# Kernel tuning notes

Measured on AMD Instinct MI355X. Metric: run time of the kernel, lower is better.

The kernel has to match this reference:

```python
import jax, jax.numpy as jnp
import numpy as np

D_MODEL = 1024
N_HEADS = 16
FEAT_DIM = 16   # q/k head dim before feature-map expansion
V_DIM = 64      # v head dim = d_model / n_heads
EPS = 1e-12


def taylor_exp(x):
    """2nd-order Taylor approx feature map of exp(q^T k / sqrt(d)).
    x: (b, h, l, d) -> (b, h, l, 1 + d + d^2)
    f(x) = [1, x / d^{1/4}, vec(x x^T) / (sqrt(2) * sqrt(d))]
    """
    d = x.shape[-1]
    rd = jnp.sqrt(jnp.float32(d))          # sqrt(d)
    rrd = jnp.sqrt(rd)                     # d^{1/4}
    r2 = jnp.sqrt(jnp.float32(2.0))
    x2 = (x[..., :, None] * x[..., None, :]).reshape(*x.shape[:-1], d * d) / r2
    ones = jnp.ones(x.shape[:-1] + (1,), dtype=x.dtype)
    return jnp.concatenate([ones, x / rrd, x2 / rd], axis=-1)


def setup_inputs() -> dict:
    key = jax.random.key(0)
    k0, k1, k2, k3, k4 = jax.random.split(key, 5)
    b, l = 2, 2048
    scale = 1.0 / np.sqrt(D_MODEL)
    return {
        "hidden_states": jax.random.normal(k0, (b, l, D_MODEL), dtype=jnp.float32),
        "Wq": jax.random.normal(k1, (D_MODEL, N_HEADS * FEAT_DIM), dtype=jnp.float32) * scale,
        "Wk": jax.random.normal(k2, (D_MODEL, N_HEADS * FEAT_DIM), dtype=jnp.float32) * scale,
        "Wv": jax.random.normal(k3, (D_MODEL, N_HEADS * V_DIM), dtype=jnp.float32) * scale,
        "Wo": jax.random.normal(k4, (N_HEADS * V_DIM, D_MODEL), dtype=jnp.float32) * scale,
    }


def reference(hidden_states, Wq, Wk, Wv, Wo):
    b, l, _ = hidden_states.shape
    # projections -> (b, h, l, d)
    q = (hidden_states @ Wq).reshape(b, l, N_HEADS, FEAT_DIM).transpose(0, 2, 1, 3)
    k = (hidden_states @ Wk).reshape(b, l, N_HEADS, FEAT_DIM).transpose(0, 2, 1, 3)
    v = (hidden_states @ Wv).reshape(b, l, N_HEADS, V_DIM).transpose(0, 2, 1, 3)

    qf = taylor_exp(q)  # (b, h, l, 273)
    kf = taylor_exp(k)

    # causal linear attention (naive parallel form used by the torch module)
    A = jnp.einsum('bhnf,bhmf->bhnm', qf, kf)
    A = jnp.tril(A)
    y = jnp.einsum('bhnm,bhme->bhne', A, v)
    # denominator: q_f . cumsum(k_f)
    z = 1.0 / (jnp.einsum('bhlf,bhlf->bhl', qf, jnp.cumsum(kf, axis=2)) + EPS)
    y = y * z[..., None]

    out = y.transpose(0, 2, 1, 3).reshape(b, l, N_HEADS * V_DIM) @ Wo
    return out
```

## Files before the change

kernel.cpp:

```cpp
#include <hip/hip_runtime.h>
#include <hip/hip_bf16.h>

#define BATCH 2
#define LSEQ 2048
#define DMODEL 1024
#define NH 16
#define DQK 16
#define DV 64
#define FDIM 273
#define CHUNK 128
#define NCH (LSEQ / CHUNK)
#define ROWS (BATCH * LSEQ)
#define NBH (BATCH * NH)
#define NBC (NBH * NCH)
#define QKVW 1536
#define C2 0.17677669529663687f

typedef short bf16x8 __attribute__((ext_vector_type(8)));
typedef float f32x4 __attribute__((ext_vector_type(4)));

__device__ __forceinline__ unsigned short f2bf(float f) {
  __hip_bfloat16 h = __float2bfloat16(f);
  unsigned short u; __builtin_memcpy(&u, &h, 2); return u;
}
__device__ __forceinline__ float bf2f(unsigned short u) {
  unsigned int v = (unsigned int)u << 16; float f; __builtin_memcpy(&f, &v, 4); return f;
}

__device__ __forceinline__ void storeC(float* C, size_t off, float v) { C[off] = v; }
__device__ __forceinline__ void storeC(unsigned short* C, size_t off, float v) {
  C[off] = f2bf(v);
}

__global__ __launch_bounds__(256) void prep(
    const float* __restrict__ hs,
    const float* __restrict__ Wq, const float* __restrict__ Wk,
    const float* __restrict__ Wv, const float* __restrict__ Wo,
    unsigned short* __restrict__ hsb,
    unsigned short* __restrict__ wqt, unsigned short* __restrict__ wkt,
    unsigned short* __restrict__ wvt, unsigned short* __restrict__ wot) {
  __shared__ float t[32][33];
  if (blockIdx.z == 4) {
    int bid = blockIdx.y * 32 + blockIdx.x;
    const float4* in4 = (const float4*)hs;
#pragma unroll
    for (int k = 0; k < 4; k++) {
      int i = bid * 1024 + k * 256 + threadIdx.x;
      float4 v = in4[i];
      ushort4 o = {f2bf(v.x), f2bf(v.y), f2bf(v.z), f2bf(v.w)};
      ((ushort4*)hsb)[i] = o;
    }
    return;
  }
  const float* W; unsigned short* Wt; int N;
  switch (blockIdx.z) {
    case 0: W = Wq; Wt = wqt; N = 256; break;
    case 1: W = Wk; Wt = wkt; N = 256; break;
    case 2: W = Wv; Wt = wvt; N = 1024; break;
    default: W = Wo; Wt = wot; N = 1024; break;
  }
  const int nb = blockIdx.x * 32;
  if (nb >= N) return;
  const int kb = blockIdx.y * 32;
  const int tx = threadIdx.x & 31, ty4 = (threadIdx.x >> 5) * 4;
#pragma unroll
  for (int r = 0; r < 4; r++)
    t[ty4 + r][tx] = W[(size_t)(kb + ty4 + r) * N + nb + tx];
  __syncthreads();
#pragma unroll
  for (int r = 0; r < 4; r++)
    Wt[(size_t)(nb + ty4 + r) * DMODEL + kb + tx] = f2bf(t[tx][ty4 + r]);
}

template <typename CT>
__global__ __launch_bounds__(256) void gemm_mfma64(
    const unsigned short* __restrict__ A, const unsigned short* __restrict__ Bt,
    CT* __restrict__ C, int M, int N, int K) {
  __shared__ unsigned short As[256 * 8];
  __shared__ unsigned short Bs[512 * 8];
  const int tid = threadIdx.x;
  const int bm = blockIdx.y * 64, bn = blockIdx.x * 128;
  const int lane = tid & 63;
  const int w = tid >> 6;
  const int qr = (w >> 1) * 32, qc = (w & 1) * 64;
  f32x4 acc[2][4] = {};

  for (int k0 = 0; k0 < K; k0 += 32) {
#pragma unroll
    for (int j = 0; j < 3; ++j) {
      int c = j * 256 + tid;
      const unsigned short* gp;
      unsigned short* lp;
      if (c < 256) {
        int cc = c;
        int row = ((cc >> 6) << 4) + (cc & 15);
        int kh = (cc >> 4) & 3;
        gp = A + (size_t)(bm + row) * K + k0 + kh * 8; lp = As + cc * 8;
      } else {
        int cc = c - 256;
        int row = ((cc >> 6) << 4) + (cc & 15);
        int kh = (cc >> 4) & 3;
        gp = Bt + (size_t)(bn + row) * K + k0 + kh * 8; lp = Bs + cc * 8;
      }
      __builtin_amdgcn_global_load_lds(
          (const __attribute__((address_space(1))) unsigned int*)(const void*)gp,
          (__attribute__((address_space(3))) unsigned int*)lp, 16, 0, 0);
    }
    __syncthreads();
    bf16x8 a[2], b[4];
#pragma unroll
    for (int i = 0; i < 2; ++i)
      a[i] = *(const bf16x8*)(As + ((qr >> 4) + i) * 512 + lane * 8);
#pragma unroll
    for (int i = 0; i < 4; ++i)
      b[i] = *(const bf16x8*)(Bs + ((qc >> 4) + i) * 512 + lane * 8);
#pragma unroll
    for (int i = 0; i < 2; ++i)
#pragma unroll
      for (int jj = 0; jj < 4; ++jj)
        acc[i][jj] = __builtin_amdgcn_mfma_f32_16x16x32_bf16(a[i], b[jj], acc[i][jj], 0, 0, 0);
    __syncthreads();
  }
  const int cn = lane & 15, r0 = (lane >> 4) * 4;
#pragma unroll
  for (int i = 0; i < 2; ++i)
#pragma unroll
    for (int jj = 0; jj < 4; ++jj) {
      size_t base = (size_t)(bm + qr + i * 16 + r0) * N + bn + qc + jj * 16 + cn;
#pragma unroll
      for (int r = 0; r < 4; ++r) storeC(C, base + (size_t)r * N, acc[i][jj][r]);
    }
}

__device__ __forceinline__ void stage_Vp(const unsigned short* __restrict__ qkvb,
                                         int row0, int h, int tid, short* Vp) {
#pragma unroll
  for (int it = 0; it < 4; it++) {
    int t = it * 256 + tid;
    int j = t >> 3, e0 = (t & 7) * 8;
    bf16x8 v8 = *(const bf16x8*)(qkvb + (size_t)(row0 + j) * QKVW + 512 + h * 64 + e0);
    int jg = j >> 3, jj = j & 7;
#pragma unroll
    for (int u = 0; u < 8; u++) {
      int e = e0 + u;
      Vp[((e >> 4) * 4 + (jg >> 2)) * 512 + ((jg & 3) * 16 + (e & 15)) * 8 + jj] =
          v8[u];
    }
  }
  {
    int n = tid & 15, jgrp = tid >> 4;
    bf16x8 v8;
#pragma unroll
    for (int u = 0; u < 8; u++) v8[u] = (n == 0) ? (short)0x3F80 : (short)0;
    *(bf16x8*)(Vp + (16 + (jgrp >> 2)) * 512 + ((jgrp & 3) * 16 + n) * 8) = v8;
  }
}

__global__ __launch_bounds__(256) void chunk_sums_mfma(
    const unsigned short* __restrict__ qkvb, unsigned short* __restrict__ Sfrag) {
  const int c = blockIdx.x, bh = blockIdx.y;
  const int b = bh >> 4, h = bh & 15;
  const int tid = threadIdx.x;
  const int lane = tid & 63, w = tid >> 6;
  const int row0 = b * LSEQ + c * CHUNK;

  __shared__ float ksT[16 * 132];
  __shared__ short SH[56 * 512];
  short* Vp = SH;
  short* Kf0 = SH + 20 * 512;
  short* Kf1 = SH + 38 * 512;

  {
    int i = tid >> 1, d0 = (tid & 1) * 8;
    bf16x8 k8 = *(const bf16x8*)(qkvb + (size_t)(row0 + i) * QKVW + 256 + h * 16 + d0);
#pragma unroll
    for (int j = 0; j < 8; j++) ksT[(d0 + j) * 132 + i] = bf2f((unsigned short)k8[j]);
  }
  stage_Vp(qkvb, row0, h, tid, Vp);
  __syncthreads();

  auto gen = [&](int kt, short* dst) {
    for (int o = tid; o < 1152; o += 256) {
      int mt = o >> 6, w6 = o & 63;
      int kh = w6 >> 4, m = w6 & 15;
      int f = mt * 16 + m;
      int i0 = kt * 32 + kh * 8;
      bf16x8 v8;
      if (f == 0) {
#pragma unroll
        for (int j = 0; j < 8; j++) v8[j] = (short)0x3F80;
      } else if (f < 17) {
        const float* ka = &ksT[(f - 1) * 132 + i0];
        float4 a0 = *(const float4*)ka, a1 = *(const float4*)(ka + 4);
        v8[0] = (short)f2bf(0.5f * a0.x); v8[1] = (short)f2bf(0.5f * a0.y);
        v8[2] = (short)f2bf(0.5f * a0.z); v8[3] = (short)f2bf(0.5f * a0.w);
        v8[4] = (short)f2bf(0.5f * a1.x); v8[5] = (short)f2bf(0.5f * a1.y);
        v8[6] = (short)f2bf(0.5f * a1.z); v8[7] = (short)f2bf(0.5f * a1.w);
      } else if (f < FDIM) {
        int ix = f - 17;
        const float* ka = &ksT[(ix >> 4) * 132 + i0];
        const float* kb2 = &ksT[(ix & 15) * 132 + i0];
        float4 a0 = *(const float4*)ka, a1 = *(const float4*)(ka + 4);
        float4 b0 = *(const float4*)kb2, b1 = *(const float4*)(kb2 + 4);
        v8[0] = (short)f2bf(C2 * a0.x * b0.x); v8[1] = (short)f2bf(C2 * a0.y * b0.y);
        v8[2] = (short)f2bf(C2 * a0.z * b0.z); v8[3] = (short)f2bf(C2 * a0.w * b0.w);
        v8[4] = (short)f2bf(C2 * a1.x * b1.x); v8[5] = (short)f2bf(C2 * a1.y * b1.y);
        v8[6] = (short)f2bf(C2 * a1.z * b1.z); v8[7] = (short)f2bf(C2 * a1.w * b1.w);
      } else {
#pragma unroll
        for (int j = 0; j < 8; j++) v8[j] = 0;
      }
      *(bf16x8*)(dst + mt * 512 + (kh * 16 + m) * 8) = v8;
    }
  };

  gen(0, Kf0);
  __syncthreads();

  f32x4 acc[5][5] = {};
  const int nmt = (w < 2) ? 5 : 4;
  for (int kt = 0; kt < 4; kt++) {
    short* cur = (kt & 1) ? Kf1 : Kf0;
    if (kt < 3) gen(kt + 1, (kt & 1) ? Kf0 : Kf1);
    bf16x8 bv[5];
#pragma unroll
    for (int nt = 0; nt < 5; nt++)
      bv[nt] = *(const bf16x8*)(Vp + (nt * 4 + kt) * 512 + lane * 8);
#pragma unroll
    for (int t2 = 0; t2 < 5; t2++) {
      if (t2 < nmt) {
        int mt = w + t2 * 4;
        bf16x8 av = *(const bf16x8*)(cur + mt * 512 + lane * 8);
#pragma unroll
        for (int nt = 0; nt < 5; nt++)
          acc[t2][nt] = __builtin_amdgcn_mfma_f32_16x16x32_bf16(av, bv[nt], acc[t2][nt], 0, 0, 0);
      }
    }
    __syncthreads();
  }

  const int cl = lane & 15, r0q = (lane >> 4) * 4;
#pragma unroll
  for (int t2 = 0; t2 < 5; t2++) {
    if (t2 < nmt) {
      int mt = w + t2 * 4;
#pragma unroll
      for (int reg = 0; reg < 4; reg++) {
        int f = mt * 16 + r0q + reg;
#pragma unroll
        for (int nt = 0; nt < 5; nt++) {
          int e = nt * 16 + cl;
          SH[((f >> 5) * 5 + nt) * 512 + (((f >> 3) & 3) * 16 + (e & 15)) * 8 + (f & 7)] =
              (short)f2bf(acc[t2][nt][reg]);
        }
      }
    }
  }
  __syncthreads();
  unsigned short* dst = Sfrag + ((size_t)bh * NCH + c) * 45 * 512;
  for (int o = tid; o < 2880; o += 256)
    *(bf16x8*)(dst + o * 8) = *(const bf16x8*)(SH + o * 8);
}

__global__ __launch_bounds__(64) void prefix_scan_frag(
    const unsigned short* __restrict__ Sfrag, unsigned short* __restrict__ PG) {
  const int kt5 = blockIdx.x, bh = blockIdx.y;
  const int lane = threadIdx.x;
  float run[8] = {0.f, 0.f, 0.f, 0.f, 0.f, 0.f, 0.f, 0.f};
  const size_t base = ((size_t)bh * NCH * 45 + kt5) * 512 + lane * 8;
#pragma unroll
  for (int cc = 0; cc < NCH; cc++) {
    size_t a = base + (size_t)cc * 45 * 512;
    bf16x8 s8 = *(const bf16x8*)(Sfrag + a);
    bf16x8 o8;
#pragma unroll
    for (int j = 0; j < 8; j++) {
      o8[j] = (short)f2bf(run[j]);
      run[j] += bf2f((unsigned short)s8[j]);
    }
    *(bf16x8*)(PG + a) = o8;
  }
}

__global__ __launch_bounds__(256) void attn_mfma(
    const unsigned short* __restrict__ qkvb, const unsigned short* __restrict__ PG,
    unsigned short* __restrict__ ybuf) {
  const int c = blockIdx.x, bh = blockIdx.y;
  const int b = bh >> 4, h = bh & 15;
  const int tid = threadIdx.x;
  const int lane = tid & 63, w = tid >> 6;
  const int row0 = b * LSEQ + c * CHUNK;

  __shared__ short U[36864];
  __shared__ float denL[128];
  unsigned short* Uu = (unsigned short*)U;

  const int qrow = (w >> 1) * 64 + lane;
  const int shalf = w & 1;
  bf16x8 qa = *(const bf16x8*)(qkvb + (size_t)(row0 + qrow) * QKVW + h * 16);
  bf16x8 qb = *(const bf16x8*)(qkvb + (size_t)(row0 + qrow) * QKVW + h * 16 + 8);

  for (int t = tid; t < 1024; t += 256) {
    int isK = t >> 9;
    int tt = t & 511;
    int i = tt >> 2, kh = tt & 3;
    bf16x8 v8 = {0, 0, 0, 0, 0, 0, 0, 0};
    if (kh < 2)
      v8 = *(const bf16x8*)(qkvb + (size_t)(row0 + i) * QKVW + isK * 256 + h * 16 + kh * 8);
    *(bf16x8*)(U + isK * 4096 + (i >> 4) * 512 + (kh * 16 + (i & 15)) * 8) = v8;
  }
  __syncthreads();

  {
    bf16x8 aq[2];
#pragma unroll
    for (int mi = 0; mi < 2; mi++)
      aq[mi] = *(const bf16x8*)(U + (w * 2 + mi) * 512 + lane * 8);
    f32x4 S[2][8] = {};
#pragma unroll
    for (int nt = 0; nt < 8; nt++) {
      bf16x8 bk = *(const bf16x8*)(U + 4096 + nt * 512 + lane * 8);
#pragma unroll
      for (int mi = 0; mi < 2; mi++)
        S[mi][nt] = __builtin_amdgcn_mfma_f32_16x16x32_bf16(aq[mi], bk, S[mi][nt], 0, 0, 0);
    }
    const int cl = lane & 15, r0q = (lane >> 4) * 4;
#pragma unroll
    for (int mi = 0; mi < 2; mi++)
#pragma unroll
      for (int nt = 0; nt < 8; nt++)
#pragma unroll
        for (int reg = 0; reg < 4; reg++) {
          int i = (w * 2 + mi) * 16 + r0q + reg;
          int j = nt * 16 + cl;
          float s = S[mi][nt][reg];
          float aij = (j <= i) ? fmaf(s, fmaf(s, 0.03125f, 0.25f), 1.0f) : 0.0f;
          U[8192 + ((i >> 4) * 4 + (j >> 5)) * 512 +
            (((j >> 3) & 3) * 16 + (i & 15)) * 8 + (j & 7)] = (short)f2bf(aij);
        }
  }
  stage_Vp(qkvb, row0, h, tid, U + 24576);
  __syncthreads();

  f32x4 Y[2][5] = {};
#pragma unroll
  for (int kc = 0; kc < 4; kc++) {
    bf16x8 a2[2];
#pragma unroll
    for (int mi = 0; mi < 2; mi++)
      a2[mi] = *(const bf16x8*)(U + 8192 + ((w * 2 + mi) * 4 + kc) * 512 + lane * 8);
#pragma unroll
    for (int nt = 0; nt < 5; nt++) {
      bf16x8 b2 = *(const bf16x8*)(U + 24576 + (nt * 4 + kc) * 512 + lane * 8);
#pragma unroll
      for (int mi = 0; mi < 2; mi++)
        Y[mi][nt] = __builtin_amdgcn_mfma_f32_16x16x32_bf16(a2[mi], b2, Y[mi][nt], 0, 0, 0);
    }
  }
  __syncthreads();

  {
    float qv[16], cq[16];
#pragma unroll
    for (int j = 0; j < 8; j++) {
      qv[j] = bf2f((unsigned short)qa[j]);
      qv[8 + j] = bf2f((unsigned short)qb[j]);
    }
#pragma unroll
    for (int j = 0; j < 16; j++) cq[j] = C2 * qv[j];
    unsigned short* qbase = Uu + (qrow >> 4) * 512 + (qrow & 15) * 8;
    if (shalf == 0) {
#pragma unroll
      for (int vk = 0; vk < 18; vk++) {
        bf16x8 v8;
#pragma unroll
        for (int j = 0; j < 8; j++) {
          int f = vk * 8 + j;
          float qf;
          if (f == 0) qf = 1.0f;
          else if (f < 17) qf = 0.5f * qv[f - 1];
          else { int ix = f - 17; qf = cq[ix >> 4] * qv[ix & 15]; }
          v8[j] = (short)f2bf(qf);
        }
        *(bf16x8*)(qbase + (vk >> 2) * 4096 + (vk & 3) * 128) = v8;
      }
    } else {
#pragma unroll
      for (int vk = 18; vk < 36; vk++) {
        bf16x8 v8;
#pragma unroll
        for (int j = 0; j < 8; j++) {
          int f = vk * 8 + j;
          float qf;
          if (f < FDIM) { int ix = f - 17; qf = cq[ix >> 4] * qv[ix & 15]; }
          else qf = 0.0f;
          v8[j] = (short)f2bf(qf);
        }
        *(bf16x8*)(qbase + (vk >> 2) * 4096 + (vk & 3) * 128) = v8;
      }
    }
  }
  __syncthreads();

  const unsigned short* pgl = PG + ((size_t)bh * NCH + c) * 45 * 512 + lane * 8;
#pragma unroll
  for (int ft = 0; ft < 9; ft++) {
    bf16x8 b3[5];
#pragma unroll
    for (int nt = 0; nt < 5; nt++)
      b3[nt] = *(const bf16x8*)(pgl + (ft * 5 + nt) * 512);
    bf16x8 a3[2];
#pragma unroll
    for (int mi = 0; mi < 2; mi++)
      a3[mi] = *(const bf16x8*)(U + ft * 4096 + (w * 2 + mi) * 512 + lane * 8);
#pragma unroll
    for (int nt = 0; nt < 5; nt++)
#pragma unroll
      for (int mi = 0; mi < 2; mi++)
        Y[mi][nt] = __builtin_amdgcn_mfma_f32_16x16x32_bf16(a3[mi], b3[nt], Y[mi][nt], 0, 0, 0);
  }

  const int cl = lane & 15, r0q = (lane >> 4) * 4;
  if (cl == 0) {
#pragma unroll
    for (int mi = 0; mi < 2; mi++)
#pragma unroll
      for (int reg = 0; reg < 4; reg++)
        denL[(w * 2 + mi) * 16 + r0q + reg] = Y[mi][4][reg];
  }
  __syncthreads();
#pragma unroll
  for (int mi = 0; mi < 2; mi++) {
    float invd[4];
#pragma unroll
    for (int reg = 0; reg < 4; reg++)
      invd[reg] = 1.0f / (denL[(w * 2 + mi) * 16 + r0q + reg] + 1e-12f);
#pragma unroll
    for (int nt = 0; nt < 4; nt++)
#pragma unroll
      for (int reg = 0; reg < 4; reg++) {
        int i = (w * 2 + mi) * 16 + r0q + reg;
        int e = nt * 16 + cl;
        ybuf[(size_t)(row0 + i) * (NH * DV) + h * DV + e] =
            f2bf(Y[mi][nt][reg] * invd[reg]);
      }
  }
}

extern "C" void kernel_launch(void* const* d_in, const int* in_sizes, int n_in,
                              void* d_out, int out_size, void* d_ws, size_t ws_size,
                              hipStream_t stream) {
  const float* hs = (const float*)d_in[0];
  const float* Wq = (const float*)d_in[1];
  const float* Wk = (const float*)d_in[2];
  const float* Wv = (const float*)d_in[3];
  const float* Wo = (const float*)d_in[4];
  float* out = (float*)d_out;

  unsigned short* qkvb  = (unsigned short*)d_ws;
  unsigned short* Sfrag = qkvb + (size_t)ROWS * QKVW;
  unsigned short* PG    = Sfrag + (size_t)NBC * 45 * 512;
  unsigned short* hsb   = PG + (size_t)NBC * 45 * 512;
  unsigned short* yb    = hsb;
  unsigned short* wqt   = hsb + (size_t)ROWS * DMODEL;
  unsigned short* wkt   = wqt + (size_t)(NH * DQK) * DMODEL;
  unsigned short* wvt   = wkt + (size_t)(NH * DQK) * DMODEL;
  unsigned short* wot   = wvt + (size_t)(NH * DV) * DMODEL;

  prep<<<dim3(32, 32, 5), 256, 0, stream>>>(hs, Wq, Wk, Wv, Wo, hsb, wqt, wkt, wvt, wot);

  gemm_mfma64<unsigned short><<<dim3(QKVW / 128, ROWS / 64), 256, 0, stream>>>(
      hsb, wqt, qkvb, ROWS, QKVW, DMODEL);

  chunk_sums_mfma<<<dim3(NCH, NBH), 256, 0, stream>>>(qkvb, Sfrag);
  prefix_scan_frag<<<dim3(45, NBH), 64, 0, stream>>>(Sfrag, PG);
  attn_mfma<<<dim3(NCH, NBH), 256, 0, stream>>>(qkvb, PG, yb);

  gemm_mfma64<float><<<dim3(DMODEL / 128, ROWS / 64), 256, 0, stream>>>(
      yb, wot, out, ROWS, DMODEL, DMODEL);
}
```

Baseline: 183.0 us.

## Pipeline GEMM with 4-stage LDS ring buffer and 128x128 tiles

Replaces the single-buffered bf16 MFMA GEMM with a 4-deep ring of LDS stages filled by async global_load_lds, using explicit vmcnt waits so loads for later k-steps overlap with MFMA work. The block tile grows from 64x128 to 128x128, so each wave now holds a 4x4 accumulator grid and fragment reuse rises. The cost is 64KB of LDS per block and half as many blocks, which lowers occupancy and grid parallelism on the small 4096-row GEMMs.

Result: faster. 168.3 us (-8.1%).

```diff
diff --git a/kernel.cpp b/kernel.cpp
--- a/kernel.cpp
+++ b/kernel.cpp
@@ -73,57 +73,71 @@
 }
 
 template <typename CT>
-__global__ __launch_bounds__(256) void gemm_mfma64(
+__global__ __launch_bounds__(256) void gemm_pipe(
     const unsigned short* __restrict__ A, const unsigned short* __restrict__ Bt,
     CT* __restrict__ C, int M, int N, int K) {
-  __shared__ unsigned short As[256 * 8];
-  __shared__ unsigned short Bs[512 * 8];
+  __shared__ unsigned short Sbuf[4 * 8192];
   const int tid = threadIdx.x;
-  const int bm = blockIdx.y * 64, bn = blockIdx.x * 128;
+  const int bm = blockIdx.y * 128, bn = blockIdx.x * 128;
   const int lane = tid & 63;
   const int w = tid >> 6;
-  const int qr = (w >> 1) * 32, qc = (w & 1) * 64;
-  f32x4 acc[2][4] = {};
-
-  for (int k0 = 0; k0 < K; k0 += 32) {
-#pragma unroll
-    for (int j = 0; j < 3; ++j) {
+  const int qr = (w >> 1) * 64, qc = (w & 1) * 64;
+  const int nk = K >> 5;
+  f32x4 acc[4][4] = {};
+
+  auto stage = [&](int t) {
+    const int k0 = t << 5;
+    unsigned short* Sb = Sbuf + (size_t)(t & 3) * 8192;
+#pragma unroll
+    for (int j = 0; j < 4; ++j) {
       int c = j * 256 + tid;
-      const unsigned short* gp;
-      unsigned short* lp;
-      if (c < 256) {
-        int cc = c;
-        int row = ((cc >> 6) << 4) + (cc & 15);
-        int kh = (cc >> 4) & 3;
-        gp = A + (size_t)(bm + row) * K + k0 + kh * 8; lp = As + cc * 8;
-      } else {
-        int cc = c - 256;
-        int row = ((cc >> 6) << 4) + (cc & 15);
-        int kh = (cc >> 4) & 3;
-        gp = Bt + (size_t)(bn + row) * K + k0 + kh * 8; lp = Bs + cc * 8;
-      }
+      int isB = c >> 9;
+      int cc = c & 511;
+      int row = ((cc >> 6) << 4) + (cc & 15);
+      int kh = (cc >> 4) & 3;
+      const unsigned short* gp =
+          (isB ? Bt + (size_t)(bn + row) * K : A + (size_t)(bm + row) * K) + k0 + kh * 8;
+      unsigned short* lp = Sb + isB * 4096 + cc * 8;
       __builtin_amdgcn_global_load_lds(
           (const __attribute__((address_space(1))) unsigned int*)(const void*)gp,
           (__attribute__((address_space(3))) unsigned int*)lp, 16, 0, 0);
     }
-    __syncthreads();
-    bf16x8 a[2], b[4];
-#pragma unroll
-    for (int i = 0; i < 2; ++i)
-      a[i] = *(const bf16x8*)(As + ((qr >> 4) + i) * 512 + lane * 8);
+  };
+
+#pragma unroll
+  for (int t = 0; t < 3; ++t)
+    if (t < nk) stage(t);
+
+  for (int t = 0; t < nk; ++t) {
+    if (t + 3 < nk) stage(t + 3);
+    if      (t + 3 < nk) asm volatile("s_waitcnt vmcnt(12)" ::: "memory");
+    else if (t + 2 < nk) asm volatile("s_waitcnt vmcnt(8)" ::: "memory");
+    else if (t + 1 < nk) asm volatile("s_waitcnt vmcnt(4)" ::: "memory");
+    else                 asm volatile("s_waitcnt vmcnt(0)" ::: "memory");
+    __builtin_amdgcn_s_barrier();
+
+    const unsigned short* Ab = Sbuf + (size_t)(t & 3) * 8192;
+    const unsigned short* Bb = Ab + 4096;
+    bf16x8 a[4], b[4];
 #pragma unroll
     for (int i = 0; i < 4; ++i)
-      b[i] = *(const bf16x8*)(Bs + ((qc >> 4) + i) * 512 + lane * 8);
-#pragma unroll
-    for (int i = 0; i < 2; ++i)
+      a[i] = *(const bf16x8*)(Ab + ((qr >> 4) + i) * 512 + lane * 8);
+#pragma unroll
+    for (int i = 0; i < 4; ++i)
+      b[i] = *(const bf16x8*)(Bb + ((qc >> 4) + i) * 512 + lane * 8);
+#pragma unroll
+    for (int i = 0; i < 4; ++i)
 #pragma unroll
       for (int jj = 0; jj < 4; ++jj)
         acc[i][jj] = __builtin_amdgcn_mfma_f32_16x16x32_bf16(a[i], b[jj], acc[i][jj], 0, 0, 0);
-    __syncthreads();
-  }
+
+    __builtin_amdgcn_s_barrier();
+    asm volatile("" ::: "memory");
+  }
+
   const int cn = lane & 15, r0 = (lane >> 4) * 4;
 #pragma unroll
-  for (int i = 0; i < 2; ++i)
+  for (int i = 0; i < 4; ++i)
 #pragma unroll
     for (int jj = 0; jj < 4; ++jj) {
       size_t base = (size_t)(bm + qr + i * 16 + r0) * N + bn + qc + jj * 16 + cn;
@@ -469,13 +483,13 @@
 
   prep<<<dim3(32, 32, 5), 256, 0, stream>>>(hs, Wq, Wk, Wv, Wo, hsb, wqt, wkt, wvt, wot);
 
-  gemm_mfma64<unsigned short><<<dim3(QKVW / 128, ROWS / 64), 256, 0, stream>>>(
+  gemm_pipe<unsigned short><<<dim3(QKVW / 128, ROWS / 128), 256, 0, stream>>>(
       hsb, wqt, qkvb, ROWS, QKVW, DMODEL);
 
   chunk_sums_mfma<<<dim3(NCH, NBH), 256, 0, stream>>>(qkvb, Sfrag);
   prefix_scan_frag<<<dim3(45, NBH), 64, 0, stream>>>(Sfrag, PG);
   attn_mfma<<<dim3(NCH, NBH), 256, 0, stream>>>(qkvb, PG, yb);
 
-  gemm_mfma64<float><<<dim3(DMODEL / 128, ROWS / 64), 256, 0, stream>>>(
+  gemm_pipe<float><<<dim3(DMODEL / 128, ROWS / 128), 256, 0, stream>>>(
       yb, wot, out, ROWS, DMODEL, DMODEL);
 }
```
